# Performance work log

Measured on AMD Instinct MI355X. Metric: run time of the kernel, lower is better.

The kernel has to match this reference:

```python
import jax, jax.numpy as jnp
import numpy as np

VOCAB_SIZE = 16384
BETA = 0.25
RESI_RATIO = 0.5  # abs(quant_resi=-0.5); kernel size 3


def setup_inputs() -> dict:
    key = jax.random.key(0)
    k1, k2, k3 = jax.random.split(key, 3)
    B, C, h, w = 16, 32, 32, 32
    f_BChw = jax.random.normal(k1, (B, C, h, w), dtype=jnp.float32)
    emb_weight = jax.random.normal(k2, (VOCAB_SIZE, C), dtype=jnp.float32)
    conv_w = jax.random.normal(k3, (C, C, 3, 3), dtype=jnp.float32) * 0.05
    conv_b = jnp.zeros((C,), dtype=jnp.float32)
    return {"f_BChw": f_BChw, "emb_weight": emb_weight, "conv_w": conv_w, "conv_b": conv_b}


def _res_conv(h_BChw, conv_w, conv_b):
    # ResConv: h*(1-r) + conv3x3(h)*r
    y = jax.lax.conv_general_dilated(
        h_BChw, conv_w, window_strides=(1, 1), padding=((1, 1), (1, 1)),
        dimension_numbers=("NCHW", "OIHW", "NCHW"))
    y = y + conv_b[None, :, None, None]
    return h_BChw * (1.0 - RESI_RATIO) + y * RESI_RATIO


def reference(f_BChw, emb_weight, conv_w, conv_b):
    f_BChw = f_BChw.astype(jnp.float32)
    B, C, h, w = f_BChw.shape
    query_NxC = jax.lax.stop_gradient(f_BChw).transpose(0, 2, 3, 1).reshape(-1, C)  # [N,C]
    # vocab_norm=False path: squared Euclidean distance via ||q||^2 + ||e||^2 - 2 q e^T
    E_dist = (jnp.sum(query_NxC * query_NxC, axis=1, keepdims=True)
              + jnp.sum(emb_weight * emb_weight, axis=1)
              - 2.0 * (query_NxC @ emb_weight.T))  # [N, vocab]
    idx_N = jnp.argmin(E_dist, axis=1)  # [N]
    # bincount for usage stats
    counts = jnp.zeros((VOCAB_SIZE,), dtype=jnp.float32).at[idx_N].add(1.0)
    # embedding gather -> [B,h,w,C] -> [B,C,h,w]
    zq_BChw = emb_weight[idx_N].reshape(B, h, w, C).transpose(0, 3, 1, 2)
    fhat_BChw = _res_conv(zq_BChw, conv_w, conv_b)
    vq_loss = (BETA * jnp.mean((jax.lax.stop_gradient(fhat_BChw) - f_BChw) ** 2)
               + jnp.mean((fhat_BChw - jax.lax.stop_gradient(f_BChw)) ** 2))
    # straight-through estimator
    fhat_out = f_BChw + jax.lax.stop_gradient(fhat_BChw - f_BChw)
    prob = counts / jnp.sum(counts)
    vocab_usage = jnp.mean((prob > 0.01 / VOCAB_SIZE).astype(jnp.float32)) * 100.0
    return fhat_out, vq_loss, vocab_usage
```

## Files before the change

kernel.cpp:

```cpp
#include <hip/hip_runtime.h>

#define VOCAB 16384
#define N_Q   16384
#define C     32
#define HW    1024
#define VCH   16
#define CODES_PER_CH 1024
#define TILES_PER_CH 64
#define GRP    8
#define NGRP   8
#define GBYTES 18432

typedef _Float16 half8 __attribute__((ext_vector_type(8)));
typedef float f32x4  __attribute__((ext_vector_type(4)));

__global__ __launch_bounds__(256) void k_prepE(const float* __restrict__ emb,
                                               char* __restrict__ Eblob,
                                               const float* __restrict__ convw,
                                               float* __restrict__ wp,
                                               unsigned long long* __restrict__ keys,
                                               int* __restrict__ counts) {
    int bx = blockIdx.x;
    if (bx >= 64) {
        if (bx == 64) {
            for (int k = threadIdx.x; k < C * C * 9; k += 256) {
                int cout = k / (C * 9);
                int r = k % (C * 9);
                int cin = r / 9;
                int tap = r % 9;
                wp[(tap * C + cin) * C + cout] = convw[k];
            }
        } else if (bx == 65) {
            for (int k = threadIdx.x; k < VOCAB; k += 256) keys[k] = ~0ULL;
        } else {
            for (int k = threadIdx.x; k < VOCAB; k += 256) counts[k] = 0;
        }
        return;
    }
    int j = bx * 256 + threadIdx.x;
    const float4* e4 = reinterpret_cast<const float4*>(emb + j * C);
    float s = 0.f;
    float v[C];
#pragma unroll
    for (int k = 0; k < 8; ++k) {
        float4 t = e4[k];
        v[4 * k] = t.x; v[4 * k + 1] = t.y; v[4 * k + 2] = t.z; v[4 * k + 3] = t.w;
        s += t.x * t.x + t.y * t.y + t.z * t.z + t.w * t.w;
    }
    float en2 = 0.5f * s;
    int tg = j >> 4, G = tg >> 3, tt = tg & 7;
    char* gb = Eblob + (size_t)G * GBYTES;
    *reinterpret_cast<float4*>(gb + 16384 + tt * 256 + (j & 15) * 16)
        = make_float4(en2, en2, en2, en2);
#pragma unroll
    for (int ko = 0; ko < 4; ++ko) {
        half8 vh, vl;
#pragma unroll
        for (int e = 0; e < 8; ++e) {
            float x = v[ko * 8 + e];
            _Float16 h = (_Float16)x;
            vh[e] = h;
            vl[e] = (_Float16)(x - (float)h);
        }
        int lane = (ko << 4) | (j & 15);
        *reinterpret_cast<half8*>(gb + tt * 1024 + lane * 16) = vh;
        *reinterpret_cast<half8*>(gb + 8192 + tt * 1024 + lane * 16) = vl;
    }
}

__device__ __forceinline__ void stage_grp(const char* gb, char* db, int w, int lane) {
#pragma unroll
    for (int k = 0; k < 5; ++k) {
        int widx = w + 4 * k;
        if (widx < 18) {
            __builtin_amdgcn_global_load_lds(
                (const __attribute__((address_space(1))) void*)(gb + widx * 1024 + lane * 16),
                (__attribute__((address_space(3))) void*)(db + widx * 1024 + lane * 16),
                16, 0, 0);
        }
    }
}

__global__ __launch_bounds__(256, 2) void k_argmin(
    const float* __restrict__ f,
    const char* __restrict__ Eblob,
    unsigned long long* __restrict__ keys) {
    __shared__ __align__(16) char lds[2 * GBYTES];
    int tid = threadIdx.x;
    int lane = tid & 63;
    int w = tid >> 6;
    int wid = blockIdx.x * 4 + w;
    int chunk = blockIdx.y;

    half8 a_hi[4], a_lo[4];
    int c0 = (lane >> 4) * 8;
#pragma unroll
    for (int qq = 0; qq < 4; ++qq) {
        int n = (wid * 4 + qq) * 16 + (lane & 15);
        int b = n >> 10, rem = n & 1023;
        const float* fp = f + (b * C + c0) * HW + rem;
#pragma unroll
        for (int e = 0; e < 8; ++e) {
            float x = -fp[e * HW];
            _Float16 h = (_Float16)x;
            a_hi[qq][e] = h;
            a_lo[qq][e] = (_Float16)(x - (float)h);
        }
    }

    float best[4][4];
#pragma unroll
    for (int qq = 0; qq < 4; ++qq)
#pragma unroll
        for (int r = 0; r < 4; ++r) best[qq][r] = __uint_as_float(0x7F800000u);

    const char* gb0 = Eblob + (size_t)(chunk * NGRP) * GBYTES;

    stage_grp(gb0, lds, w, lane);
    __syncthreads();

    unsigned mpack = 0xFFFFFFC0u;
    asm("" : "+v"(mpack));

    for (int g = 0; g < NGRP; ++g) {
        if (g + 1 < NGRP)
            stage_grp(gb0 + (size_t)(g + 1) * GBYTES, lds + ((g + 1) & 1) * GBYTES, w, lane);
        const char* bbl = lds + (g & 1) * GBYTES + lane * 16;
        const char* ebl = lds + (g & 1) * GBYTES + 16384 + (lane & 15) * 16;
        unsigned tbase = (unsigned)(g * GRP);
#pragma unroll
        for (int tt = 0; tt < GRP; ++tt) {
            half8 bh = *(const half8*)(bbl + tt * 1024);
            half8 bl = *(const half8*)(bbl + 8192 + tt * 1024);
            f32x4 eq = *(const f32x4*)(ebl + tt * 256);
            unsigned t = tbase + (unsigned)tt;
#pragma unroll
            for (int qq = 0; qq < 4; ++qq) {
                f32x4 acc = __builtin_amdgcn_mfma_f32_16x16x32_f16(a_hi[qq], bh, eq, 0, 0, 0);
                acc = __builtin_amdgcn_mfma_f32_16x16x32_f16(a_hi[qq], bl, acc, 0, 0, 0);
                acc = __builtin_amdgcn_mfma_f32_16x16x32_f16(a_lo[qq], bh, acc, 0, 0, 0);
#pragma unroll
                for (int r = 0; r < 4; ++r) {
                    unsigned p = (__float_as_uint(acc[r]) & mpack) | t;
                    best[qq][r] = fminf(best[qq][r], __uint_as_float(p));
                }
            }
        }
        __syncthreads();
    }

#pragma unroll
    for (int qq = 0; qq < 4; ++qq)
#pragma unroll
        for (int r = 0; r < 4; ++r) {
            float d = best[qq][r];
            int t = (int)(__float_as_uint(d) & 63u);
            int code = chunk * CODES_PER_CH + (t << 4) + (lane & 15);
#pragma unroll
            for (int m = 1; m < 16; m <<= 1) {
                float od = __shfl_xor(d, m, 64);
                int oc = __shfl_xor(code, m, 64);
                if (od < d || (od == d && oc < code)) { d = od; code = oc; }
            }
            if ((lane & 15) == 0) {
                int row = ((lane >> 4) * 4) + r;
                int n = (wid * 4 + qq) * 16 + row;
                unsigned bits = __float_as_uint(d);
                unsigned s = ((int)bits >= 0) ? (bits | 0x80000000u) : ~bits;
                unsigned long long key = ((unsigned long long)s << 32) | (unsigned)code;
                atomicMin(&keys[n], key);
            }
        }
}

__global__ __launch_bounds__(256) void k_conv(const unsigned long long* __restrict__ keys,
                                              const float* __restrict__ emb,
                                              const float* __restrict__ wp,
                                              const float* __restrict__ bias,
                                              const float* __restrict__ f,
                                              int* __restrict__ counts,
                                              float* __restrict__ out,
                                              float* __restrict__ lpart) {
    __shared__ float sZ[128 * 33];
    __shared__ float sW[9216];
    __shared__ float red[256];
    int blk = blockIdx.x;
    int b = blk >> 4;
    int r0 = (blk & 15) * 2;
    int tid = threadIdx.x;

    {
        float4* dW = reinterpret_cast<float4*>(sW);
        const float4* sWp = reinterpret_cast<const float4*>(wp);
        for (int i = tid; i < 2304; i += 256) dW[i] = sWp[i];
    }
    {
        int px = tid >> 1, half = tid & 1;
        int row = px >> 5, col = px & 31;
        int gy = r0 - 1 + row;
        float* d = &sZ[px * 33 + half * 16];
        if (gy >= 0 && gy < 32) {
            int id = (int)(keys[b * HW + gy * 32 + col] & 0xFFFFFFFFULL);
            const float4* s = reinterpret_cast<const float4*>(emb + id * C + half * 16);
#pragma unroll
            for (int k = 0; k < 4; ++k) {
                float4 v = s[k];
                d[4 * k] = v.x; d[4 * k + 1] = v.y; d[4 * k + 2] = v.z; d[4 * k + 3] = v.w;
            }
        } else {
#pragma unroll
            for (int k = 0; k < 16; ++k) d[k] = 0.f;
        }
    }
    __syncthreads();

    int tx = tid & 31, ty = (tid >> 5) & 1, cg = tid >> 6;
    int co0 = cg * 8;
    int gy = r0 + ty;
    if (cg == 0) {
        int id = (int)(keys[b * HW + gy * 32 + tx] & 0xFFFFFFFFULL);
        atomicAdd(&counts[id], 1);
    }
    float acc[8];
#pragma unroll
    for (int u = 0; u < 8; ++u) acc[u] = bias[co0 + u];
    for (int dy = -1; dy <= 1; ++dy) {
        for (int dx = -1; dx <= 1; ++dx) {
            int gx = tx + dx;
            if (gx < 0 || gx >= 32) continue;
            const float* zp = &sZ[((ty + 1 + dy) * 32 + gx) * 33];
            int tap = (dy + 1) * 3 + (dx + 1);
            const float* wtap = &sW[tap * C * C + co0];
#pragma unroll
            for (int cin = 0; cin < C; ++cin) {
                float z = zp[cin];
                const f32x4* w4 = reinterpret_cast<const f32x4*>(wtap + cin * C);
                f32x4 wa = w4[0], wb = w4[1];
#pragma unroll
                for (int u = 0; u < 4; ++u) acc[u] = fmaf(z, wa[u], acc[u]);
#pragma unroll
                for (int u = 0; u < 4; ++u) acc[4 + u] = fmaf(z, wb[u], acc[4 + u]);
            }
        }
    }
    float lsum = 0.f;
#pragma unroll
    for (int u = 0; u < 8; ++u) {
        int cc = co0 + u;
        float zqv = sZ[((ty + 1) * 32 + tx) * 33 + cc];
        float fh = 0.5f * (zqv + acc[u]);
        int off = (b * C + cc) * HW + gy * 32 + tx;
        out[off] = fh;
        float diff = fh - f[off];
        lsum += diff * diff;
    }
    red[tid] = lsum;
    __syncthreads();
    for (int s = 128; s > 0; s >>= 1) {
        if (tid < s) red[tid] += red[tid + s];
        __syncthreads();
    }
    if (tid == 0) lpart[blk] = red[0];
}

__global__ __launch_bounds__(256) void k_final(const float* __restrict__ lpart,
                                               const int* __restrict__ counts,
                                               float* __restrict__ out) {
    __shared__ float red[256];
    __shared__ int redi[256];
    int tid = threadIdx.x;
    int used = 0;
    for (int i = tid; i < VOCAB; i += 256) used += (counts[i] != 0) ? 1 : 0;
    red[tid] = lpart[tid];
    redi[tid] = used;
    __syncthreads();
    for (int s = 128; s > 0; s >>= 1) {
        if (tid < s) { red[tid] += red[tid + s]; redi[tid] += redi[tid + s]; }
        __syncthreads();
    }
    if (tid == 0) {
        out[N_Q * C]     = 1.25f * red[0] / (float)(N_Q * C);
        out[N_Q * C + 1] = 100.f * (float)redi[0] / (float)VOCAB;
    }
}

extern "C" void kernel_launch(void* const* d_in, const int* in_sizes, int n_in,
                              void* d_out, int out_size, void* d_ws, size_t ws_size,
                              hipStream_t stream) {
    const float* f     = (const float*)d_in[0];
    const float* emb   = (const float*)d_in[1];
    const float* convw = (const float*)d_in[2];
    const float* convb = (const float*)d_in[3];
    float* out = (float*)d_out;
    float* ws  = (float*)d_ws;

    float*  wp     = ws;
    float*  lpart  = ws + 9216;
    int*    counts = (int*)(ws + 9472);
    unsigned long long* keys = (unsigned long long*)(ws + 25856);
    char*   Eblob  = (char*)(ws + 58624);

    k_prepE<<<67, 256, 0, stream>>>(emb, Eblob, convw, wp, keys, counts);
    dim3 g2(64, VCH);
    k_argmin<<<g2, 256, 0, stream>>>(f, Eblob, keys);
    k_conv<<<256, 256, 0, stream>>>(keys, emb, wp, convb, f, counts, out, lpart);
    k_final<<<1, 256, 0, stream>>>(lpart, counts, out);
}
```

Baseline: 89.93 us.

## Halve argmin staging group size and fold final reduction into conv kernel

The argmin kernel now stages 4 codebook tiles per LDS group instead of 8, with 16 groups per chunk. This halves the LDS footprint per block and raises the launch-bounds occupancy hint from 2 to 6 blocks, so more waves can hide load latency, at the cost of more barriers and staging rounds. Separately, the final loss and usage reduction kernel is removed: the last conv block to finish, detected with a device-scope atomic counter, performs it. This saves one kernel launch but adds a serialized tail inside k_conv.

Measured after the change: 201.4 us. 124% more time.

```diff
diff --git a/kernel.cpp b/kernel.cpp
--- a/kernel.cpp
+++ b/kernel.cpp
@@ -6,10 +6,9 @@
 #define HW    1024
 #define VCH   16
 #define CODES_PER_CH 1024
-#define TILES_PER_CH 64
-#define GRP    8
-#define NGRP   8
-#define GBYTES 18432
+#define GRP    4
+#define NGRP   16
+#define GBYTES 9216
 
 typedef _Float16 half8 __attribute__((ext_vector_type(8)));
 typedef float f32x4  __attribute__((ext_vector_type(4)));
@@ -19,7 +18,8 @@
                                                const float* __restrict__ convw,
                                                float* __restrict__ wp,
                                                unsigned long long* __restrict__ keys,
-                                               int* __restrict__ counts) {
+                                               int* __restrict__ counts,
+                                               int* __restrict__ done) {
     int bx = blockIdx.x;
     if (bx >= 64) {
         if (bx == 64) {
@@ -34,6 +34,7 @@
             for (int k = threadIdx.x; k < VOCAB; k += 256) keys[k] = ~0ULL;
         } else {
             for (int k = threadIdx.x; k < VOCAB; k += 256) counts[k] = 0;
+            if (threadIdx.x == 0) *done = 0;
         }
         return;
     }
@@ -48,9 +49,9 @@
         s += t.x * t.x + t.y * t.y + t.z * t.z + t.w * t.w;
     }
     float en2 = 0.5f * s;
-    int tg = j >> 4, G = tg >> 3, tt = tg & 7;
+    int tg = j >> 4, G = tg >> 2, tt = tg & 3;
     char* gb = Eblob + (size_t)G * GBYTES;
-    *reinterpret_cast<float4*>(gb + 16384 + tt * 256 + (j & 15) * 16)
+    *reinterpret_cast<float4*>(gb + 8192 + tt * 256 + (j & 15) * 16)
         = make_float4(en2, en2, en2, en2);
 #pragma unroll
     for (int ko = 0; ko < 4; ++ko) {
@@ -64,15 +65,15 @@
         }
         int lane = (ko << 4) | (j & 15);
         *reinterpret_cast<half8*>(gb + tt * 1024 + lane * 16) = vh;
-        *reinterpret_cast<half8*>(gb + 8192 + tt * 1024 + lane * 16) = vl;
+        *reinterpret_cast<half8*>(gb + 4096 + tt * 1024 + lane * 16) = vl;
     }
 }
 
 __device__ __forceinline__ void stage_grp(const char* gb, char* db, int w, int lane) {
 #pragma unroll
-    for (int k = 0; k < 5; ++k) {
+    for (int k = 0; k < 3; ++k) {
         int widx = w + 4 * k;
-        if (widx < 18) {
+        if (widx < 9) {
             __builtin_amdgcn_global_load_lds(
                 (const __attribute__((address_space(1))) void*)(gb + widx * 1024 + lane * 16),
                 (__attribute__((address_space(3))) void*)(db + widx * 1024 + lane * 16),
@@ -81,7 +82,7 @@
     }
 }
 
-__global__ __launch_bounds__(256, 2) void k_argmin(
+__global__ __launch_bounds__(256, 6) void k_argmin(
     const float* __restrict__ f,
     const char* __restrict__ Eblob,
     unsigned long long* __restrict__ keys) {
@@ -126,12 +127,12 @@
         if (g + 1 < NGRP)
             stage_grp(gb0 + (size_t)(g + 1) * GBYTES, lds + ((g + 1) & 1) * GBYTES, w, lane);
         const char* bbl = lds + (g & 1) * GBYTES + lane * 16;
-        const char* ebl = lds + (g & 1) * GBYTES + 16384 + (lane & 15) * 16;
+        const char* ebl = lds + (g & 1) * GBYTES + 8192 + (lane & 15) * 16;
         unsigned tbase = (unsigned)(g * GRP);
 #pragma unroll
         for (int tt = 0; tt < GRP; ++tt) {
             half8 bh = *(const half8*)(bbl + tt * 1024);
-            half8 bl = *(const half8*)(bbl + 8192 + tt * 1024);
+            half8 bl = *(const half8*)(bbl + 4096 + tt * 1024);
             f32x4 eq = *(const f32x4*)(ebl + tt * 256);
             unsigned t = tbase + (unsigned)tt;
 #pragma unroll
@@ -180,10 +181,12 @@
                                               const float* __restrict__ f,
                                               int* __restrict__ counts,
                                               float* __restrict__ out,
-                                              float* __restrict__ lpart) {
+                                              float* __restrict__ lpart,
+                                              int* __restrict__ done) {
     __shared__ float sZ[128 * 33];
     __shared__ float sW[9216];
     __shared__ float red[256];
+    __shared__ int sfin;
     int blk = blockIdx.x;
     int b = blk >> 4;
     int r0 = (blk & 15) * 2;
@@ -261,26 +264,29 @@
         __syncthreads();
     }
     if (tid == 0) lpart[blk] = red[0];
-}
-
-__global__ __launch_bounds__(256) void k_final(const float* __restrict__ lpart,
-                                               const int* __restrict__ counts,
-                                               float* __restrict__ out) {
-    __shared__ float red[256];
-    __shared__ int redi[256];
-    int tid = threadIdx.x;
-    int used = 0;
-    for (int i = tid; i < VOCAB; i += 256) used += (counts[i] != 0) ? 1 : 0;
-    red[tid] = lpart[tid];
-    redi[tid] = used;
+
+    if (tid == 0) {
+        __threadfence();
+        int v = atomicAdd(done, 1);
+        sfin = (v == 255) ? 1 : 0;
+    }
     __syncthreads();
-    for (int s = 128; s > 0; s >>= 1) {
-        if (tid < s) { red[tid] += red[tid + s]; redi[tid] += redi[tid + s]; }
+    if (sfin) {
+        __threadfence();
+        int* redi = (int*)sZ;
+        int used = 0;
+        for (int i = tid; i < VOCAB; i += 256) used += (counts[i] != 0) ? 1 : 0;
+        red[tid] = lpart[tid];
+        redi[tid] = used;
         __syncthreads();
-    }
-    if (tid == 0) {
-        out[N_Q * C]     = 1.25f * red[0] / (float)(N_Q * C);
-        out[N_Q * C + 1] = 100.f * (float)redi[0] / (float)VOCAB;
+        for (int s = 128; s > 0; s >>= 1) {
+            if (tid < s) { red[tid] += red[tid + s]; redi[tid] += redi[tid + s]; }
+            __syncthreads();
+        }
+        if (tid == 0) {
+            out[N_Q * C]     = 1.25f * red[0] / (float)(N_Q * C);
+            out[N_Q * C + 1] = 100.f * (float)redi[0] / (float)VOCAB;
+        }
     }
 }
 
@@ -296,13 +302,13 @@
 
     float*  wp     = ws;
     float*  lpart  = ws + 9216;
-    int*    counts = (int*)(ws + 9472);
-    unsigned long long* keys = (unsigned long long*)(ws + 25856);
-    char*   Eblob  = (char*)(ws + 58624);
-
-    k_prepE<<<67, 256, 0, stream>>>(emb, Eblob, convw, wp, keys, counts);
+    int*    done   = (int*)(ws + 9472);
+    int*    counts = (int*)(ws + 9488);
+    unsigned long long* keys = (unsigned long long*)(ws + 25872);
+    char*   Eblob  = (char*)(ws + 58640);
+
+    k_prepE<<<67, 256, 0, stream>>>(emb, Eblob, convw, wp, keys, counts, done);
     dim3 g2(64, VCH);
     k_argmin<<<g2, 256, 0, stream>>>(f, Eblob, keys);
-    k_conv<<<256, 256, 0, stream>>>(keys, emb, wp, convb, f, counts, out, lpart);
-    k_final<<<1, 256, 0, stream>>>(lpart, counts, out);
-}
+    k_conv<<<256, 256, 0, stream>>>(keys, emb, wp, convb, f, counts, out, lpart, done);
+}
```
